# Kernel optimization log

Measured on AMD Instinct MI355X. Metric: run time of the kernel, lower is better.

The kernel has to match this reference:

```python
import jax, jax.numpy as jnp
import numpy as np

N = 100000   # nodes
E = 1600000  # edges
F_IN = 256   # input features
H = 128      # hidden
C = 40       # classes


def setup_inputs() -> dict:
    key = jax.random.key(0)
    ks = jax.random.split(key, 6)
    x = jax.random.normal(ks[0], (N, F_IN), dtype=jnp.float32)
    edge_index = jax.random.randint(ks[1], (2, E), 0, N, dtype=jnp.int32)
    edge_attr = jax.random.uniform(ks[2], (E,), dtype=jnp.float32)
    # Glorot-style init like GCNConv
    W1 = jax.random.normal(ks[3], (F_IN, H), dtype=jnp.float32) * (1.0 / np.sqrt(F_IN))
    b1 = jnp.zeros((H,), dtype=jnp.float32)
    W2 = jax.random.normal(ks[4], (H, C), dtype=jnp.float32) * (1.0 / np.sqrt(H))
    b2 = jnp.zeros((C,), dtype=jnp.float32)
    return {"x": x, "edge_index": edge_index, "edge_attr": edge_attr,
            "W1": W1, "b1": b1, "W2": W2, "b2": b2}


def _gcn_norm(edge_index, edge_weight, num_nodes):
    # PyG gcn_norm: add self-loops (weight 1), symmetric D^{-1/2} A D^{-1/2}
    row, col = edge_index[0], edge_index[1]
    loop = jnp.arange(num_nodes, dtype=row.dtype)
    row = jnp.concatenate([row, loop])
    col = jnp.concatenate([col, loop])
    ew = jnp.concatenate([edge_weight, jnp.ones((num_nodes,), edge_weight.dtype)])
    deg = jax.ops.segment_sum(ew, col, num_segments=num_nodes)
    dinv = jnp.where(deg > 0, jax.lax.rsqrt(deg), 0.0)
    norm = dinv[row] * ew * dinv[col]
    return row, col, norm


def _gcn_conv(x, row, col, norm, W, b):
    h = x @ W                              # [N, out] dense transform first
    msg = h[row] * norm[:, None]           # gather source + edge scaling
    out = jax.ops.segment_sum(msg, col, num_segments=x.shape[0])  # scatter-add
    return out + b


def reference(x, edge_index, edge_attr, W1, b1, W2, b2):
    row, col, norm = _gcn_norm(edge_index, edge_attr, x.shape[0])
    h = _gcn_conv(x, row, col, norm, W1, b1)
    h = jax.nn.relu(h)
    # dropout is identity in eval mode
    h = _gcn_conv(h, row, col, norm, W2, b2)
    return jax.nn.log_softmax(h, axis=1)
```

## Files before the change

### kernel.cpp

```cpp
#include <hip/hip_runtime.h>

#define N_NODES 100000
#define N_EDGES 1600000
#define F_INPUT 256
#define H_DIM   128
#define C_DIM   40
#define NB1     ((N_NODES + 255) / 256)
#define NGEMM1  1563
#define NCOUNT  6250
#define NMEGA   (NGEMM1 + NCOUNT)

typedef short  bf8   __attribute__((ext_vector_type(8)));
typedef float  f32x4 __attribute__((ext_vector_type(4)));
typedef float  f32x2 __attribute__((ext_vector_type(2)));
typedef unsigned short u16x8 __attribute__((ext_vector_type(8)));

static __device__ __forceinline__ unsigned short f2bf(float f) {
    union { float f; unsigned u; } v; v.f = f;
    unsigned r = v.u + 0x7FFFu + ((v.u >> 16) & 1u);
    return (unsigned short)(r >> 16);
}
static __device__ __forceinline__ float bf2f(unsigned short b) {
    union { unsigned u; float f; } v; v.u = ((unsigned)b) << 16;
    return v.f;
}
static __device__ __forceinline__ f32x2 bfpair(unsigned u) {
    union { unsigned u; float f; } lo, hi;
    lo.u = u << 16; hi.u = u & 0xFFFF0000u;
    return (f32x2){lo.f, hi.f};
}

__global__ void k_pre(unsigned* packed, const float* __restrict__ W1,
                      const float* __restrict__ W2,
                      unsigned short* Wp1, unsigned short* Wp2) {
    if (blockIdx.x < NB1) {
        int i = blockIdx.x * 256 + threadIdx.x;
        if (i < N_NODES) packed[i] = (1u << 16);
        return;
    }
    int idx = (blockIdx.x - NB1) * 256 + threadIdx.x;
    if (idx < 32768) {
        int j = idx & 7, lane = (idx >> 3) & 63, ks = (idx >> 9) & 7, nt = idx >> 12;
        int m = lane & 15, q = lane >> 4;
        Wp1[idx] = f2bf(W1[(ks * 32 + q * 8 + j) * H_DIM + nt * 16 + m]);
    }
    int idx2 = idx - 32768;
    if (idx2 >= 0 && idx2 < 6144) {
        int j = idx2 & 7, lane = (idx2 >> 3) & 63, ks = (idx2 >> 9) & 3, nt = idx2 >> 11;
        int m = lane & 15, q = lane >> 4;
        int n = nt * 16 + m;
        Wp2[idx2] = (n < C_DIM) ? f2bf(W2[(ks * 32 + q * 8 + j) * C_DIM + n]) : (unsigned short)0;
    }
}

__global__ __launch_bounds__(256, 4) void k_mega(
        const float* __restrict__ x, const unsigned short* __restrict__ Wp,
        unsigned short* __restrict__ h,
        const int* __restrict__ col, const float* __restrict__ ea,
        unsigned* packed, int* __restrict__ rank) {
    __shared__ unsigned short lds_out[64 * H_DIM];
    int b = blockIdx.x;
    bool is_gemm = (b % 5 == 0);
    if (!is_gemm) {
        int cb = b - b / 5 - 1;
        int e = cb * 256 + threadIdx.x;
        if (e < N_EDGES) {
            int c = col[e];
            unsigned q = __float2uint_rn(ea[e] * 65536.0f);
            unsigned old = atomicAdd(packed + c, (1u << 24) | q);
            rank[e] = (int)(old >> 24);
        }
        return;
    }
    int tile = b / 5;
    int tid = threadIdx.x;
    int wave = tid >> 6, lane = tid & 63;
    int m = lane & 15, q = lane >> 4;
    int row0 = tile * 64 + wave * 16;
    int rowA = row0 + m; if (rowA >= N_NODES) rowA = N_NODES - 1;

    f32x4 acc[8];
#pragma unroll
    for (int i = 0; i < 8; i++) acc[i] = (f32x4){0.f, 0.f, 0.f, 0.f};
    const float* xr = x + (long)rowA * F_INPUT + q * 8;
#pragma unroll
    for (int ks = 0; ks < 8; ks++) {
        float4 a0 = *(const float4*)(xr + ks * 32);
        float4 a1 = *(const float4*)(xr + ks * 32 + 4);
        bf8 a;
        a[0] = (short)f2bf(a0.x); a[1] = (short)f2bf(a0.y);
        a[2] = (short)f2bf(a0.z); a[3] = (short)f2bf(a0.w);
        a[4] = (short)f2bf(a1.x); a[5] = (short)f2bf(a1.y);
        a[6] = (short)f2bf(a1.z); a[7] = (short)f2bf(a1.w);
#pragma unroll
        for (int nt = 0; nt < 8; nt++) {
            bf8 bb = *(const bf8*)(Wp + (((nt * 8 + ks) * 64 + lane) << 3));
            acc[nt] = __builtin_amdgcn_mfma_f32_16x16x32_bf16(a, bb, acc[nt], 0, 0, 0);
        }
    }
    int lrow = wave * 16 + q * 4;
#pragma unroll
    for (int nt = 0; nt < 8; nt++)
#pragma unroll
        for (int r = 0; r < 4; r++)
            lds_out[(lrow + r) * H_DIM + nt * 16 + m] = f2bf(acc[nt][r]);
    __syncthreads();
    int valid = N_NODES - tile * 64; if (valid > 64) valid = 64;
    unsigned short* gbase = h + (size_t)tile * 64 * H_DIM;
#pragma unroll
    for (int i = 0; i < 4; i++) {
        int idx = (i * 256 + tid) * 8;
        if (idx < valid * H_DIM)
            *(u16x8*)(gbase + idx) = *(const u16x8*)(lds_out + idx);
    }
}

__global__ void k_scan1(const unsigned* __restrict__ packed, int* start, int* bsum,
                        float* dinv) {
    __shared__ int s[256];
    int i = blockIdx.x * 256 + threadIdx.x;
    unsigned pk = (i < N_NODES) ? packed[i] : 0;
    if (i < N_NODES) dinv[i] = rsqrtf((float)(pk & 0xFFFFFFu) * (1.0f / 65536.0f));
    int v = (int)(pk >> 24);
    s[threadIdx.x] = v; __syncthreads();
    for (int off = 1; off < 256; off <<= 1) {
        int t = (threadIdx.x >= off) ? s[threadIdx.x - off] : 0;
        __syncthreads();
        s[threadIdx.x] += t;
        __syncthreads();
    }
    if (i < N_NODES) start[i] = s[threadIdx.x] - v;
    if (threadIdx.x == 255) bsum[blockIdx.x] = s[255];
}

__global__ void k_scan2(int* bsum) {
    __shared__ int s[512];
    int v = (threadIdx.x < NB1) ? bsum[threadIdx.x] : 0;
    s[threadIdx.x] = v; __syncthreads();
    for (int off = 1; off < 512; off <<= 1) {
        int t = (threadIdx.x >= off) ? s[threadIdx.x - off] : 0;
        __syncthreads();
        s[threadIdx.x] += t;
        __syncthreads();
    }
    if (threadIdx.x < NB1) bsum[threadIdx.x] = s[threadIdx.x] - v;
}

__global__ void k_scatter(const int* __restrict__ row, const int* __restrict__ col,
                          const float* __restrict__ ea, const float* __restrict__ dinv,
                          const int* __restrict__ start, const int* __restrict__ bsum,
                          const int* __restrict__ rank, int2* __restrict__ csr) {
    int e = blockIdx.x * 256 + threadIdx.x;
    if (e < N_EDGES) {
        int c = col[e];
        int r = row[e];
        int pos = start[c] + bsum[c >> 8] + rank[e];
        float w = ea[e] * dinv[r];
        csr[pos] = make_int2(r, __float_as_int(w));
    }
}

__global__ void k_agg1(const unsigned short* __restrict__ h, const int2* __restrict__ csr,
                       const int* __restrict__ start, const int* __restrict__ bsum,
                       const unsigned* __restrict__ packed,
                       const float* __restrict__ dinv, const float* __restrict__ b1,
                       unsigned short* __restrict__ h1) {
    int c = (blockIdx.x * blockDim.x + threadIdx.x) >> 6;
    int lane = threadIdx.x & 63;
    if (c >= N_NODES) return;
    int eg = lane >> 4, cl = lane & 15;
    float di = dinv[c];
    int s = start[c] + bsum[c >> 8];
    int n = (int)(packed[c] >> 24);

    float w[5]; int r[5];
#pragma unroll
    for (int t = 0; t < 5; t++) {
        int i = eg + 4 * t;
        int2 p = csr[s + ((i < n) ? i : 0)];
        bool val = (i < n);
        r[t] = val ? p.x : c;
        w[t] = val ? __int_as_float(p.y) : 0.f;
    }
    uint4 gv[5];
#pragma unroll
    for (int t = 0; t < 5; t++)
        gv[t] = *(const uint4*)(h + (long)r[t] * H_DIM + cl * 8);
    uint4 selfv = (eg == 0) ? *(const uint4*)(h + (long)c * H_DIM + cl * 8)
                            : (uint4){0, 0, 0, 0};

    f32x2 acc[4];
#pragma unroll
    for (int k = 0; k < 4; k++) acc[k] = (f32x2){0.f, 0.f};
    {
        unsigned sv[4] = {selfv.x, selfv.y, selfv.z, selfv.w};
        f32x2 dd = (f32x2){di, di};
        if (eg == 0)
#pragma unroll
            for (int k = 0; k < 4; k++) acc[k] += dd * bfpair(sv[k]);
    }
#pragma unroll
    for (int t = 0; t < 5; t++) {
        unsigned vv[4] = {gv[t].x, gv[t].y, gv[t].z, gv[t].w};
        f32x2 ww = (f32x2){w[t], w[t]};
#pragma unroll
        for (int k = 0; k < 4; k++) acc[k] += ww * bfpair(vv[k]);
    }
    for (int i = 20 + eg; i < n; i += 4) {
        int2 p = csr[s + i];
        uint4 v4 = *(const uint4*)(h + (long)p.x * H_DIM + cl * 8);
        unsigned vv[4] = {v4.x, v4.y, v4.z, v4.w};
        float wt = __int_as_float(p.y);
        f32x2 ww = (f32x2){wt, wt};
#pragma unroll
        for (int k = 0; k < 4; k++) acc[k] += ww * bfpair(vv[k]);
    }
#pragma unroll
    for (int k = 0; k < 4; k++) {
        acc[k].x += __shfl_xor(acc[k].x, 16); acc[k].y += __shfl_xor(acc[k].y, 16);
        acc[k].x += __shfl_xor(acc[k].x, 32); acc[k].y += __shfl_xor(acc[k].y, 32);
    }
    if (eg == 0) {
        u16x8 o;
#pragma unroll
        for (int k = 0; k < 4; k++) {
            o[2 * k]     = f2bf(fmaxf(di * acc[k].x + b1[cl * 8 + 2 * k], 0.f));
            o[2 * k + 1] = f2bf(fmaxf(di * acc[k].y + b1[cl * 8 + 2 * k + 1], 0.f));
        }
        *(u16x8*)(h1 + (long)c * H_DIM + cl * 8) = o;
    }
}

__global__ __launch_bounds__(256, 4) void k_gemm2(const unsigned short* __restrict__ h1,
                        const unsigned short* __restrict__ Wp,
                        unsigned short* __restrict__ h2) {
    __shared__ unsigned short lds_out[64 * C_DIM];
    int tid = threadIdx.x;
    int wave = tid >> 6, lane = tid & 63;
    int m = lane & 15, q = lane >> 4;
    int row0 = blockIdx.x * 64 + wave * 16;
    int rowA = row0 + m; if (rowA >= N_NODES) rowA = N_NODES - 1;

    f32x4 acc[3];
#pragma unroll
    for (int i = 0; i < 3; i++) acc[i] = (f32x4){0.f, 0.f, 0.f, 0.f};
    const unsigned short* hr = h1 + (long)rowA * H_DIM + q * 8;
#pragma unroll
    for (int ks = 0; ks < 4; ks++) {
        bf8 a = *(const bf8*)(hr + ks * 32);
#pragma unroll
        for (int nt = 0; nt < 3; nt++) {
            bf8 b = *(const bf8*)(Wp + (((nt * 4 + ks) * 64 + lane) << 3));
            acc[nt] = __builtin_amdgcn_mfma_f32_16x16x32_bf16(a, b, acc[nt], 0, 0, 0);
        }
    }
    int lrow = wave * 16 + q * 4;
#pragma unroll
    for (int nt = 0; nt < 3; nt++)
#pragma unroll
        for (int r = 0; r < 4; r++) {
            int colo = nt * 16 + m;
            if (colo < C_DIM)
                lds_out[(lrow + r) * C_DIM + colo] = f2bf(acc[nt][r]);
        }
    __syncthreads();
    int valid = N_NODES - blockIdx.x * 64; if (valid > 64) valid = 64;
    unsigned short* gbase = h2 + (size_t)blockIdx.x * 64 * C_DIM;
    int total = valid * C_DIM;
#pragma unroll
    for (int i = 0; i < 3; i++) {
        int idx = (i * 256 + tid) * 4;
        if (idx < total)
            *(uint2*)(gbase + idx) = *(const uint2*)(lds_out + idx);
    }
}

__global__ void k_agg2(const unsigned short* __restrict__ h2, const int2* __restrict__ csr,
                       const int* __restrict__ start, const int* __restrict__ bsum,
                       const unsigned* __restrict__ packed,
                       const float* __restrict__ dinv, const float* __restrict__ b2,
                       float* __restrict__ out) {
    int c = (blockIdx.x * blockDim.x + threadIdx.x) >> 6;
    int lane = threadIdx.x & 63;
    if (c >= N_NODES) return;
    int eg = lane >> 3, cl = lane & 7;
    float di = dinv[c];
    int s = start[c] + bsum[c >> 8];
    int n = (int)(packed[c] >> 24);

    float w[3]; int r[3];
#pragma unroll
    for (int t = 0; t < 3; t++) {
        int i = eg + 8 * t;
        int2 p = csr[s + ((i < n) ? i : 0)];
        bool val = (i < n);
        r[t] = val ? p.x : c;
        w[t] = val ? __int_as_float(p.y) : 0.f;
    }
    uint4 gv[3] = {{0,0,0,0},{0,0,0,0},{0,0,0,0}};
    uint4 selfv = {0, 0, 0, 0};
    if (cl < 5) {
#pragma unroll
        for (int t = 0; t < 3; t++)
            gv[t] = *(const uint4*)(h2 + (long)r[t] * C_DIM + cl * 8);
        if (eg == 0) selfv = *(const uint4*)(h2 + (long)c * C_DIM + cl * 8);
    }
    f32x2 acc[4];
#pragma unroll
    for (int k = 0; k < 4; k++) acc[k] = (f32x2){0.f, 0.f};
    {
        unsigned sv[4] = {selfv.x, selfv.y, selfv.z, selfv.w};
        f32x2 dd = (f32x2){di, di};
        if (eg == 0 && cl < 5)
#pragma unroll
            for (int k = 0; k < 4; k++) acc[k] += dd * bfpair(sv[k]);
    }
#pragma unroll
    for (int t = 0; t < 3; t++) {
        unsigned vv[4] = {gv[t].x, gv[t].y, gv[t].z, gv[t].w};
        f32x2 ww = (f32x2){w[t], w[t]};
#pragma unroll
        for (int k = 0; k < 4; k++) acc[k] += ww * bfpair(vv[k]);
    }
    for (int i = 24 + eg; i < n; i += 8) {
        int2 p = csr[s + i];
        if (cl < 5) {
            uint4 v4 = *(const uint4*)(h2 + (long)p.x * C_DIM + cl * 8);
            unsigned vv[4] = {v4.x, v4.y, v4.z, v4.w};
            float wt = __int_as_float(p.y);
            f32x2 ww = (f32x2){wt, wt};
#pragma unroll
            for (int k = 0; k < 4; k++) acc[k] += ww * bfpair(vv[k]);
        }
    }
#pragma unroll
    for (int k = 0; k < 4; k++) {
        acc[k].x += __shfl_xor(acc[k].x, 8);  acc[k].y += __shfl_xor(acc[k].y, 8);
        acc[k].x += __shfl_xor(acc[k].x, 16); acc[k].y += __shfl_xor(acc[k].y, 16);
        acc[k].x += __shfl_xor(acc[k].x, 32); acc[k].y += __shfl_xor(acc[k].y, 32);
    }
    float v[8];
    float lm = -INFINITY;
    if (cl < 5) {
#pragma unroll
        for (int k = 0; k < 4; k++) {
            v[2 * k]     = di * acc[k].x + b2[cl * 8 + 2 * k];
            v[2 * k + 1] = di * acc[k].y + b2[cl * 8 + 2 * k + 1];
            lm = fmaxf(lm, fmaxf(v[2 * k], v[2 * k + 1]));
        }
    }
    lm = fmaxf(lm, __shfl_xor(lm, 1));
    lm = fmaxf(lm, __shfl_xor(lm, 2));
    lm = fmaxf(lm, __shfl_xor(lm, 4));
    float ls = 0.f;
    if (cl < 5) {
#pragma unroll
        for (int j = 0; j < 8; j++) ls += __expf(v[j] - lm);
    }
    ls += __shfl_xor(ls, 1);
    ls += __shfl_xor(ls, 2);
    ls += __shfl_xor(ls, 4);
    if (eg == 0 && cl < 5) {
        float lsm = lm + logf(ls);
        f32x4 o0, o1;
#pragma unroll
        for (int j = 0; j < 4; j++) { o0[j] = v[j] - lsm; o1[j] = v[j + 4] - lsm; }
        *(f32x4*)(out + (long)c * C_DIM + cl * 8)     = o0;
        *(f32x4*)(out + (long)c * C_DIM + cl * 8 + 4) = o1;
    }
}

extern "C" void kernel_launch(void* const* d_in, const int* in_sizes, int n_in,
                              void* d_out, int out_size, void* d_ws, size_t ws_size,
                              hipStream_t stream) {
    const float* x  = (const float*)d_in[0];
    const int*   ei = (const int*)d_in[1];
    const float* ea = (const float*)d_in[2];
    const float* W1 = (const float*)d_in[3];
    const float* b1 = (const float*)d_in[4];
    const float* W2 = (const float*)d_in[5];
    const float* b2 = (const float*)d_in[6];
    const int* row = ei;
    const int* col = ei + N_EDGES;

    char* ws = (char*)d_ws;
    size_t off = 0;
    auto alloc = [&](size_t bytes) -> void* {
        void* p = ws + off;
        off = (off + bytes + 255) & ~(size_t)255;
        return p;
    };
    unsigned*       packed = (unsigned*)alloc((size_t)N_NODES * 4);
    float*          dinv   = (float*)alloc((size_t)N_NODES * 4);
    int*            rank   = (int*)alloc((size_t)N_EDGES * 4);
    int*            start  = (int*)alloc((size_t)N_NODES * 4);
    int*            bsum   = (int*)alloc(512 * 4);
    int2*           csr    = (int2*)alloc((size_t)N_EDGES * 8);
    unsigned short* Wp1    = (unsigned short*)alloc(32768 * 2);
    unsigned short* Wp2    = (unsigned short*)alloc(6144 * 2);
    unsigned short* h      = (unsigned short*)alloc((size_t)(N_NODES + 64) * H_DIM * 2);
    unsigned short* h1     = (unsigned short*)alloc((size_t)N_NODES * H_DIM * 2);
    unsigned short* h2     = (unsigned short*)alloc((size_t)(N_NODES + 64) * C_DIM * 2);

    k_pre<<<NB1 + 152, 256, 0, stream>>>(packed, W1, W2, Wp1, Wp2);
    k_mega<<<NMEGA, 256, 0, stream>>>(x, Wp1, h, col, ea, packed, rank);
    k_scan1<<<NB1, 256, 0, stream>>>(packed, start, bsum, dinv);
    k_scan2<<<1, 512, 0, stream>>>(bsum);
    k_scatter<<<N_EDGES / 256, 256, 0, stream>>>(row, col, ea, dinv, start, bsum, rank, csr);
    k_agg1<<<N_NODES / 4, 256, 0, stream>>>(h, csr, start, bsum, packed, dinv, b1, h1);
    k_gemm2<<<(N_NODES + 63) / 64, 256, 0, stream>>>(h1, Wp2, h2);
    k_agg2<<<N_NODES / 4, 256, 0, stream>>>(h2, csr, start, bsum, packed, dinv, b2, (float*)d_out);
}
```

Baseline: 402.7 us.

## Pad atomic counters to cache-line stride and batch edge atomics per thread

Each node's packed degree/count atomic now sits in its own 128-byte slot, so concurrent atomics to nearby nodes no longer contend on shared cache lines. Count blocks now handle four edges per thread and interleave 1:1 with GEMM blocks, issuing several independent atomics per thread. A compact cnt array is written in scan1 so the aggregation kernels avoid reading the strided buffer. The cost is a 32x larger packed buffer (about 12.8 MB) to initialize and read with strided access.

Result: slower. 430.8 us (+7.0%).

```diff
diff --git a/kernel.cpp b/kernel.cpp
--- a/kernel.cpp
+++ b/kernel.cpp
@@ -7,8 +7,9 @@
 #define C_DIM   40
 #define NB1     ((N_NODES + 255) / 256)
 #define NGEMM1  1563
-#define NCOUNT  6250
+#define NCOUNT  1563
 #define NMEGA   (NGEMM1 + NCOUNT)
+#define PSTR    32
 
 typedef short  bf8   __attribute__((ext_vector_type(8)));
 typedef float  f32x4 __attribute__((ext_vector_type(4)));
@@ -35,7 +36,7 @@
                       unsigned short* Wp1, unsigned short* Wp2) {
     if (blockIdx.x < NB1) {
         int i = blockIdx.x * 256 + threadIdx.x;
-        if (i < N_NODES) packed[i] = (1u << 16);
+        if (i < N_NODES) packed[(size_t)i * PSTR] = (1u << 16);
         return;
     }
     int idx = (blockIdx.x - NB1) * 256 + threadIdx.x;
@@ -60,19 +61,31 @@
         unsigned* packed, int* __restrict__ rank) {
     __shared__ unsigned short lds_out[64 * H_DIM];
     int b = blockIdx.x;
-    bool is_gemm = (b % 5 == 0);
+    bool is_gemm = ((b & 1) == 0);
     if (!is_gemm) {
-        int cb = b - b / 5 - 1;
-        int e = cb * 256 + threadIdx.x;
-        if (e < N_EDGES) {
-            int c = col[e];
-            unsigned q = __float2uint_rn(ea[e] * 65536.0f);
-            unsigned old = atomicAdd(packed + c, (1u << 24) | q);
-            rank[e] = (int)(old >> 24);
+        int cb = b >> 1;
+        int e0 = cb * 1024 + threadIdx.x;
+        int cs[4]; unsigned qs[4]; unsigned old[4];
+#pragma unroll
+        for (int k = 0; k < 4; k++) {
+            int e = e0 + k * 256;
+            if (e < N_EDGES) {
+                cs[k] = col[e];
+                qs[k] = __float2uint_rn(ea[e] * 65536.0f);
+            } else cs[k] = -1;
+        }
+#pragma unroll
+        for (int k = 0; k < 4; k++)
+            if (cs[k] >= 0)
+                old[k] = atomicAdd(packed + (size_t)cs[k] * PSTR, (1u << 24) | qs[k]);
+#pragma unroll
+        for (int k = 0; k < 4; k++) {
+            int e = e0 + k * 256;
+            if (e < N_EDGES) rank[e] = (int)(old[k] >> 24);
         }
         return;
     }
-    int tile = b / 5;
+    int tile = b >> 1;
     int tid = threadIdx.x;
     int wave = tid >> 6, lane = tid & 63;
     int m = lane & 15, q = lane >> 4;
@@ -116,11 +129,14 @@
 }
 
 __global__ void k_scan1(const unsigned* __restrict__ packed, int* start, int* bsum,
-                        float* dinv) {
+                        float* dinv, int* __restrict__ cnt) {
     __shared__ int s[256];
     int i = blockIdx.x * 256 + threadIdx.x;
-    unsigned pk = (i < N_NODES) ? packed[i] : 0;
-    if (i < N_NODES) dinv[i] = rsqrtf((float)(pk & 0xFFFFFFu) * (1.0f / 65536.0f));
+    unsigned pk = (i < N_NODES) ? packed[(size_t)i * PSTR] : 0;
+    if (i < N_NODES) {
+        dinv[i] = rsqrtf((float)(pk & 0xFFFFFFu) * (1.0f / 65536.0f));
+        cnt[i] = (int)(pk >> 24);
+    }
     int v = (int)(pk >> 24);
     s[threadIdx.x] = v; __syncthreads();
     for (int off = 1; off < 256; off <<= 1) {
@@ -162,7 +178,7 @@
 
 __global__ void k_agg1(const unsigned short* __restrict__ h, const int2* __restrict__ csr,
                        const int* __restrict__ start, const int* __restrict__ bsum,
-                       const unsigned* __restrict__ packed,
+                       const int* __restrict__ cnt,
                        const float* __restrict__ dinv, const float* __restrict__ b1,
                        unsigned short* __restrict__ h1) {
     int c = (blockIdx.x * blockDim.x + threadIdx.x) >> 6;
@@ -171,7 +187,7 @@
     int eg = lane >> 4, cl = lane & 15;
     float di = dinv[c];
     int s = start[c] + bsum[c >> 8];
-    int n = (int)(packed[c] >> 24);
+    int n = cnt[c];
 
     float w[5]; int r[5];
 #pragma unroll
@@ -277,7 +293,7 @@
 
 __global__ void k_agg2(const unsigned short* __restrict__ h2, const int2* __restrict__ csr,
                        const int* __restrict__ start, const int* __restrict__ bsum,
-                       const unsigned* __restrict__ packed,
+                       const int* __restrict__ cnt,
                        const float* __restrict__ dinv, const float* __restrict__ b2,
                        float* __restrict__ out) {
     int c = (blockIdx.x * blockDim.x + threadIdx.x) >> 6;
@@ -286,7 +302,7 @@
     int eg = lane >> 3, cl = lane & 7;
     float di = dinv[c];
     int s = start[c] + bsum[c >> 8];
-    int n = (int)(packed[c] >> 24);
+    int n = cnt[c];
 
     float w[3]; int r[3];
 #pragma unroll
@@ -390,11 +406,12 @@
         off = (off + bytes + 255) & ~(size_t)255;
         return p;
     };
-    unsigned*       packed = (unsigned*)alloc((size_t)N_NODES * 4);
+    unsigned*       packed = (unsigned*)alloc((size_t)N_NODES * PSTR * 4);
     float*          dinv   = (float*)alloc((size_t)N_NODES * 4);
     int*            rank   = (int*)alloc((size_t)N_EDGES * 4);
     int*            start  = (int*)alloc((size_t)N_NODES * 4);
     int*            bsum   = (int*)alloc(512 * 4);
+    int*            cnt    = (int*)alloc((size_t)N_NODES * 4);
     int2*           csr    = (int2*)alloc((size_t)N_EDGES * 8);
     unsigned short* Wp1    = (unsigned short*)alloc(32768 * 2);
     unsigned short* Wp2    = (unsigned short*)alloc(6144 * 2);
@@ -404,10 +421,10 @@
 
     k_pre<<<NB1 + 152, 256, 0, stream>>>(packed, W1, W2, Wp1, Wp2);
     k_mega<<<NMEGA, 256, 0, stream>>>(x, Wp1, h, col, ea, packed, rank);
-    k_scan1<<<NB1, 256, 0, stream>>>(packed, start, bsum, dinv);
+    k_scan1<<<NB1, 256, 0, stream>>>(packed, start, bsum, dinv, cnt);
     k_scan2<<<1, 512, 0, stream>>>(bsum);
     k_scatter<<<N_EDGES / 256, 256, 0, stream>>>(row, col, ea, dinv, start, bsum, rank, csr);
-    k_agg1<<<N_NODES / 4, 256, 0, stream>>>(h, csr, start, bsum, packed, dinv, b1, h1);
+    k_agg1<<<N_NODES / 4, 256, 0, stream>>>(h, csr, start, bsum, cnt, dinv, b1, h1);
     k_gemm2<<<(N_NODES + 63) / 64, 256, 0, stream>>>(h1, Wp2, h2);
-    k_agg2<<<N_NODES / 4, 256, 0, stream>>>(h2, csr, start, bsum, packed, dinv, b2, (float*)d_out);
-}
+    k_agg2<<<N_NODES / 4, 256, 0, stream>>>(h2, csr, start, bsum, cnt, dinv, b2, (float*)d_out);
+}
```

## Privatize degree-count atomics per XCD to avoid cross-die atomic traffic

Applied to the files above, without the earlier changes.

Gives each XCD its own copy of the packed degree/weight counters, read via the XCC_ID hardware register, and issues the atomics at workgroup scope so they can resolve in the local L2 instead of at device scope. The scan kernel merges the eight copies into a total count, a weight sum and per-XCD prefix offsets, which the scatter kernel uses to place edges. This trades more init memory (8x counters) and extra reads in the scan and scatter kernels for cheaper atomics. Workgroup scope on per-XCD arrays depends on blocks on the same XCD sharing coherent L2, which the code assumes.

New measurement: 412.9 us. +2.5%, slower.

```diff
diff --git a/kernel.cpp b/kernel.cpp
--- a/kernel.cpp
+++ b/kernel.cpp
@@ -6,6 +6,7 @@
 #define H_DIM   128
 #define C_DIM   40
 #define NB1     ((N_NODES + 255) / 256)
+#define NB8     ((8 * N_NODES + 255) / 256)
 #define NGEMM1  1563
 #define NCOUNT  6250
 #define NMEGA   (NGEMM1 + NCOUNT)
@@ -29,16 +30,21 @@
     lo.u = u << 16; hi.u = u & 0xFFFF0000u;
     return (f32x2){lo.f, hi.f};
 }
-
-__global__ void k_pre(unsigned* packed, const float* __restrict__ W1,
+static __device__ __forceinline__ unsigned xcc_id() {
+    unsigned x;
+    asm volatile("s_getreg_b32 %0, hwreg(HW_REG_XCC_ID)" : "=s"(x));
+    return x & 7u;
+}
+
+__global__ void k_pre(unsigned* packed8, const float* __restrict__ W1,
                       const float* __restrict__ W2,
                       unsigned short* Wp1, unsigned short* Wp2) {
-    if (blockIdx.x < NB1) {
+    if (blockIdx.x < NB8) {
         int i = blockIdx.x * 256 + threadIdx.x;
-        if (i < N_NODES) packed[i] = (1u << 16);
+        if (i < 8 * N_NODES) packed8[i] = (i < N_NODES) ? (1u << 16) : 0u;
         return;
     }
-    int idx = (blockIdx.x - NB1) * 256 + threadIdx.x;
+    int idx = (blockIdx.x - NB8) * 256 + threadIdx.x;
     if (idx < 32768) {
         int j = idx & 7, lane = (idx >> 3) & 63, ks = (idx >> 9) & 7, nt = idx >> 12;
         int m = lane & 15, q = lane >> 4;
@@ -57,7 +63,7 @@
         const float* __restrict__ x, const unsigned short* __restrict__ Wp,
         unsigned short* __restrict__ h,
         const int* __restrict__ col, const float* __restrict__ ea,
-        unsigned* packed, int* __restrict__ rank) {
+        unsigned* packed8, int* __restrict__ rank) {
     __shared__ unsigned short lds_out[64 * H_DIM];
     int b = blockIdx.x;
     bool is_gemm = (b % 5 == 0);
@@ -67,8 +73,11 @@
         if (e < N_EDGES) {
             int c = col[e];
             unsigned q = __float2uint_rn(ea[e] * 65536.0f);
-            unsigned old = atomicAdd(packed + c, (1u << 24) | q);
-            rank[e] = (int)(old >> 24);
+            unsigned xcd = xcc_id();
+            unsigned old = __hip_atomic_fetch_add(
+                packed8 + (size_t)xcd * N_NODES + c, (1u << 24) | q,
+                __ATOMIC_RELAXED, __HIP_MEMORY_SCOPE_WORKGROUP);
+            rank[e] = (int)((old >> 24) | (xcd << 8));
         }
         return;
     }
@@ -115,13 +124,28 @@
     }
 }
 
-__global__ void k_scan1(const unsigned* __restrict__ packed, int* start, int* bsum,
-                        float* dinv) {
+__global__ void k_scan1(const unsigned* __restrict__ packed8, int* start, int* bsum,
+                        float* dinv, int* __restrict__ cnt, uint2* __restrict__ xoff) {
     __shared__ int s[256];
     int i = blockIdx.x * 256 + threadIdx.x;
-    unsigned pk = (i < N_NODES) ? packed[i] : 0;
-    if (i < N_NODES) dinv[i] = rsqrtf((float)(pk & 0xFFFFFFu) * (1.0f / 65536.0f));
-    int v = (int)(pk >> 24);
+    int v = 0;
+    if (i < N_NODES) {
+        unsigned wsum = 0, run = 0;
+        unsigned lo = 0, hi = 0;
+#pragma unroll
+        for (int xc = 0; xc < 8; xc++) {
+            unsigned pk = packed8[(size_t)xc * N_NODES + i];
+            unsigned c = pk >> 24;
+            wsum += pk & 0xFFFFFFu;
+            if (xc < 4) lo |= (run & 0xFFu) << (8 * xc);
+            else        hi |= (run & 0xFFu) << (8 * (xc - 4));
+            run += c;
+        }
+        dinv[i] = rsqrtf((float)wsum * (1.0f / 65536.0f));
+        cnt[i] = (int)run;
+        xoff[i] = make_uint2(lo, hi);
+        v = (int)run;
+    }
     s[threadIdx.x] = v; __syncthreads();
     for (int off = 1; off < 256; off <<= 1) {
         int t = (threadIdx.x >= off) ? s[threadIdx.x - off] : 0;
@@ -149,12 +173,18 @@
 __global__ void k_scatter(const int* __restrict__ row, const int* __restrict__ col,
                           const float* __restrict__ ea, const float* __restrict__ dinv,
                           const int* __restrict__ start, const int* __restrict__ bsum,
-                          const int* __restrict__ rank, int2* __restrict__ csr) {
+                          const int* __restrict__ rank, const uint2* __restrict__ xoff,
+                          int2* __restrict__ csr) {
     int e = blockIdx.x * 256 + threadIdx.x;
     if (e < N_EDGES) {
         int c = col[e];
         int r = row[e];
-        int pos = start[c] + bsum[c >> 8] + rank[e];
+        int rk = rank[e];
+        int xcd = rk >> 8, r0 = rk & 0xFF;
+        uint2 xo = xoff[c];
+        unsigned w32 = (xcd & 4) ? xo.y : xo.x;
+        int off = (int)((w32 >> (8 * (xcd & 3))) & 0xFFu);
+        int pos = start[c] + bsum[c >> 8] + off + r0;
         float w = ea[e] * dinv[r];
         csr[pos] = make_int2(r, __float_as_int(w));
     }
@@ -162,7 +192,7 @@
 
 __global__ void k_agg1(const unsigned short* __restrict__ h, const int2* __restrict__ csr,
                        const int* __restrict__ start, const int* __restrict__ bsum,
-                       const unsigned* __restrict__ packed,
+                       const int* __restrict__ cnt,
                        const float* __restrict__ dinv, const float* __restrict__ b1,
                        unsigned short* __restrict__ h1) {
     int c = (blockIdx.x * blockDim.x + threadIdx.x) >> 6;
@@ -171,7 +201,7 @@
     int eg = lane >> 4, cl = lane & 15;
     float di = dinv[c];
     int s = start[c] + bsum[c >> 8];
-    int n = (int)(packed[c] >> 24);
+    int n = cnt[c];
 
     float w[5]; int r[5];
 #pragma unroll
@@ -277,7 +307,7 @@
 
 __global__ void k_agg2(const unsigned short* __restrict__ h2, const int2* __restrict__ csr,
                        const int* __restrict__ start, const int* __restrict__ bsum,
-                       const unsigned* __restrict__ packed,
+                       const int* __restrict__ cnt,
                        const float* __restrict__ dinv, const float* __restrict__ b2,
                        float* __restrict__ out) {
     int c = (blockIdx.x * blockDim.x + threadIdx.x) >> 6;
@@ -286,7 +316,7 @@
     int eg = lane >> 3, cl = lane & 7;
     float di = dinv[c];
     int s = start[c] + bsum[c >> 8];
-    int n = (int)(packed[c] >> 24);
+    int n = cnt[c];
 
     float w[3]; int r[3];
 #pragma unroll
@@ -390,24 +420,26 @@
         off = (off + bytes + 255) & ~(size_t)255;
         return p;
     };
-    unsigned*       packed = (unsigned*)alloc((size_t)N_NODES * 4);
-    float*          dinv   = (float*)alloc((size_t)N_NODES * 4);
-    int*            rank   = (int*)alloc((size_t)N_EDGES * 4);
-    int*            start  = (int*)alloc((size_t)N_NODES * 4);
-    int*            bsum   = (int*)alloc(512 * 4);
-    int2*           csr    = (int2*)alloc((size_t)N_EDGES * 8);
-    unsigned short* Wp1    = (unsigned short*)alloc(32768 * 2);
-    unsigned short* Wp2    = (unsigned short*)alloc(6144 * 2);
-    unsigned short* h      = (unsigned short*)alloc((size_t)(N_NODES + 64) * H_DIM * 2);
-    unsigned short* h1     = (unsigned short*)alloc((size_t)N_NODES * H_DIM * 2);
-    unsigned short* h2     = (unsigned short*)alloc((size_t)(N_NODES + 64) * C_DIM * 2);
-
-    k_pre<<<NB1 + 152, 256, 0, stream>>>(packed, W1, W2, Wp1, Wp2);
-    k_mega<<<NMEGA, 256, 0, stream>>>(x, Wp1, h, col, ea, packed, rank);
-    k_scan1<<<NB1, 256, 0, stream>>>(packed, start, bsum, dinv);
+    unsigned*       packed8 = (unsigned*)alloc((size_t)8 * N_NODES * 4);
+    float*          dinv    = (float*)alloc((size_t)N_NODES * 4);
+    int*            rank    = (int*)alloc((size_t)N_EDGES * 4);
+    int*            start   = (int*)alloc((size_t)N_NODES * 4);
+    int*            bsum    = (int*)alloc(512 * 4);
+    int*            cnt     = (int*)alloc((size_t)N_NODES * 4);
+    uint2*          xoff    = (uint2*)alloc((size_t)N_NODES * 8);
+    int2*           csr     = (int2*)alloc((size_t)N_EDGES * 8);
+    unsigned short* Wp1     = (unsigned short*)alloc(32768 * 2);
+    unsigned short* Wp2     = (unsigned short*)alloc(6144 * 2);
+    unsigned short* h       = (unsigned short*)alloc((size_t)(N_NODES + 64) * H_DIM * 2);
+    unsigned short* h1      = (unsigned short*)alloc((size_t)N_NODES * H_DIM * 2);
+    unsigned short* h2      = (unsigned short*)alloc((size_t)(N_NODES + 64) * C_DIM * 2);
+
+    k_pre<<<NB8 + 152, 256, 0, stream>>>(packed8, W1, W2, Wp1, Wp2);
+    k_mega<<<NMEGA, 256, 0, stream>>>(x, Wp1, h, col, ea, packed8, rank);
+    k_scan1<<<NB1, 256, 0, stream>>>(packed8, start, bsum, dinv, cnt, xoff);
     k_scan2<<<1, 512, 0, stream>>>(bsum);
-    k_scatter<<<N_EDGES / 256, 256, 0, stream>>>(row, col, ea, dinv, start, bsum, rank, csr);
-    k_agg1<<<N_NODES / 4, 256, 0, stream>>>(h, csr, start, bsum, packed, dinv, b1, h1);
+    k_scatter<<<N_EDGES / 256, 256, 0, stream>>>(row, col, ea, dinv, start, bsum, rank, xoff, csr);
+    k_agg1<<<N_NODES / 4, 256, 0, stream>>>(h, csr, start, bsum, cnt, dinv, b1, h1);
     k_gemm2<<<(N_NODES + 63) / 64, 256, 0, stream>>>(h1, Wp2, h2);
-    k_agg2<<<N_NODES / 4, 256, 0, stream>>>(h2, csr, start, bsum, packed, dinv, b2, (float*)d_out);
-}
+    k_agg2<<<N_NODES / 4, 256, 0, stream>>>(h2, csr, start, bsum, cnt, dinv, b2, (float*)d_out);
+}
```
